# Kernel optimization log

Measured on AMD Instinct MI355X. Metric: run time of the kernel, lower is better.

The kernel has to match this reference:

```python
import jax, jax.numpy as jnp
import numpy as np

N_NODES = 50000
D_FEAT = 128
N_EDGES = 800000
C = 1.0  # curvature (init kwarg)
MIN_NORM = 1e-15
ARTANH_EPS = 1e-15


def logmap0(x, c):
    # PoincareBall.logmap0: x/(sqrt(c)||x||) * artanh(sqrt(c)||x||), with the
    # same clamping as the torch repo (norm clamped to MIN_NORM, artanh arg to 1-eps).
    sqrt_c = c ** 0.5
    x_norm = jnp.maximum(jnp.linalg.norm(x, axis=-1, keepdims=True), MIN_NORM)
    u = jnp.clip(sqrt_c * x_norm, -1.0 + ARTANH_EPS, 1.0 - ARTANH_EPS)
    return x * (jnp.arctanh(u) / (sqrt_c * x_norm))


def setup_inputs() -> dict:
    key = jax.random.key(0)
    k1, k2, k3, k4 = jax.random.split(key, 4)
    # scale into the Poincare ball (||x|| < 1/sqrt(c))
    x = jax.random.normal(k1, (N_NODES, D_FEAT), dtype=jnp.float32) * 1e-3
    adj_rows = jax.random.randint(k2, (N_EDGES,), 0, N_NODES, dtype=jnp.int32)
    adj_cols = jax.random.randint(k3, (N_EDGES,), 0, N_NODES, dtype=jnp.int32)
    adj_vals = jax.random.uniform(k4, (N_EDGES,), dtype=jnp.float32)
    return {"x": x, "adj_rows": adj_rows, "adj_cols": adj_cols, "adj_vals": adj_vals}


def reference(x, adj_rows, adj_cols, adj_vals) -> jnp.ndarray:
    x_tangent = logmap0(x, C)                       # [N, d] elementwise hyperbolic map
    gathered = adj_vals[:, None] * x_tangent[adj_cols]  # [E, d] edge-parallel gather
    support_t = jax.ops.segment_sum(gathered, adj_rows, num_segments=N_NODES)  # [N, d]
    return support_t
```

## Files before the change

kernel.cpp:

```cpp
#include <hip/hip_runtime.h>
#include <math.h>

#define D_FEAT 128
#define CAP 64
#define OCAP 1024

static __device__ inline unsigned short f2bf(float f) {
    unsigned u = __float_as_uint(f);
    u += 0x7FFFu + ((u >> 16) & 1u);
    return (unsigned short)(u >> 16);
}

__global__ void scatter_scale_kernel(const float* __restrict__ x,
                                     unsigned short* __restrict__ xt,
                                     const int* __restrict__ rows,
                                     const int* __restrict__ cols,
                                     const float* __restrict__ vals,
                                     int* __restrict__ cnt,
                                     int2* __restrict__ buckets,
                                     int* __restrict__ ocount,
                                     int4* __restrict__ oedges,
                                     int n_nodes, int n_edges,
                                     int n_scatter_blocks) {
    if ((int)blockIdx.x < n_scatter_blocks) {
        const int xcd = blockIdx.x & 7;
        const int chunk = blockIdx.x >> 3;
        int base = chunk * 1024 + threadIdx.x;
        #pragma unroll
        for (int k = 0; k < 4; ++k) {
            int e = base + k * 256;
            if (e < n_edges) {
                int r = rows[e];
                if ((r & 7) == xcd) {
                    int slot = atomicAdd(&cnt[r], 1);
                    int2 p;
                    p.x = cols[e];
                    p.y = __float_as_int(vals[e]);
                    if (slot < CAP) {
                        buckets[(size_t)r * CAP + slot] = p;
                    } else {
                        int o = atomicAdd(ocount, 1);
                        if (o < OCAP) {
                            int4 q; q.x = r; q.y = p.x; q.z = p.y; q.w = 0;
                            oedges[o] = q;
                        }
                    }
                }
            }
        }
    } else {
        const int lane = threadIdx.x & 63;
        const int wave = threadIdx.x >> 6;
        const int row = ((int)blockIdx.x - n_scatter_blocks) * 4 + wave;
        if (row >= n_nodes) return;

        const float2* xr = (const float2*)(x + (size_t)row * D_FEAT);
        float2 v = xr[lane];
        float ss = v.x * v.x + v.y * v.y;
        #pragma unroll
        for (int off = 32; off > 0; off >>= 1)
            ss += __shfl_xor(ss, off, 64);

        float norm = sqrtf(ss);
        float nc = fmaxf(norm, 1e-15f);
        float u = fminf(nc, 1.0f - 1e-15f);
        float at = 0.5f * (log1pf(u) - log1pf(-u));
        float s = at / nc;

        ushort2 o;
        o.x = f2bf(v.x * s);
        o.y = f2bf(v.y * s);
        ((ushort2*)(xt + (size_t)row * D_FEAT))[lane] = o;
    }
}

__global__ void gather_bucket_kernel(const unsigned short* __restrict__ xt,
                                     const int* __restrict__ cnt,
                                     const int2* __restrict__ buckets,
                                     float* __restrict__ out, int n_nodes) {
    const int lane = threadIdx.x & 63;
    const int wave = threadIdx.x >> 6;
    const int xcd = blockIdx.x & 7;
    const int idx = blockIdx.x >> 3;
    const int m = idx * 4 + wave;
    const int row = xcd + (m << 3);
    if (row >= n_nodes) return;

    int deg = cnt[row];
    deg = deg < CAP ? deg : CAP;

    int2 myp = {0, 0};
    if (lane < deg) myp = buckets[(size_t)row * CAP + lane];
    int pc = myp.x;
    float pw = __int_as_float(myp.y);

    float accx = 0.0f, accy = 0.0f;
    int j = 0;
    for (; j + 8 <= deg; j += 8) {
        int c0 = __shfl(pc, j, 64),     c1 = __shfl(pc, j + 1, 64);
        int c2 = __shfl(pc, j + 2, 64), c3 = __shfl(pc, j + 3, 64);
        int c4 = __shfl(pc, j + 4, 64), c5 = __shfl(pc, j + 5, 64);
        int c6 = __shfl(pc, j + 6, 64), c7 = __shfl(pc, j + 7, 64);
        float w0 = __shfl(pw, j, 64),     w1 = __shfl(pw, j + 1, 64);
        float w2 = __shfl(pw, j + 2, 64), w3 = __shfl(pw, j + 3, 64);
        float w4 = __shfl(pw, j + 4, 64), w5 = __shfl(pw, j + 5, 64);
        float w6 = __shfl(pw, j + 6, 64), w7 = __shfl(pw, j + 7, 64);
        unsigned u0 = ((const unsigned*)(xt + ((size_t)c0 << 7)))[lane];
        unsigned u1 = ((const unsigned*)(xt + ((size_t)c1 << 7)))[lane];
        unsigned u2 = ((const unsigned*)(xt + ((size_t)c2 << 7)))[lane];
        unsigned u3 = ((const unsigned*)(xt + ((size_t)c3 << 7)))[lane];
        unsigned u4 = ((const unsigned*)(xt + ((size_t)c4 << 7)))[lane];
        unsigned u5 = ((const unsigned*)(xt + ((size_t)c5 << 7)))[lane];
        unsigned u6 = ((const unsigned*)(xt + ((size_t)c6 << 7)))[lane];
        unsigned u7 = ((const unsigned*)(xt + ((size_t)c7 << 7)))[lane];
        accx = fmaf(w0, __uint_as_float(u0 << 16), accx);
        accy = fmaf(w0, __uint_as_float(u0 & 0xFFFF0000u), accy);
        accx = fmaf(w1, __uint_as_float(u1 << 16), accx);
        accy = fmaf(w1, __uint_as_float(u1 & 0xFFFF0000u), accy);
        accx = fmaf(w2, __uint_as_float(u2 << 16), accx);
        accy = fmaf(w2, __uint_as_float(u2 & 0xFFFF0000u), accy);
        accx = fmaf(w3, __uint_as_float(u3 << 16), accx);
        accy = fmaf(w3, __uint_as_float(u3 & 0xFFFF0000u), accy);
        accx = fmaf(w4, __uint_as_float(u4 << 16), accx);
        accy = fmaf(w4, __uint_as_float(u4 & 0xFFFF0000u), accy);
        accx = fmaf(w5, __uint_as_float(u5 << 16), accx);
        accy = fmaf(w5, __uint_as_float(u5 & 0xFFFF0000u), accy);
        accx = fmaf(w6, __uint_as_float(u6 << 16), accx);
        accy = fmaf(w6, __uint_as_float(u6 & 0xFFFF0000u), accy);
        accx = fmaf(w7, __uint_as_float(u7 << 16), accx);
        accy = fmaf(w7, __uint_as_float(u7 & 0xFFFF0000u), accy);
    }
    for (; j + 4 <= deg; j += 4) {
        int c0 = __shfl(pc, j, 64),     c1 = __shfl(pc, j + 1, 64);
        int c2 = __shfl(pc, j + 2, 64), c3 = __shfl(pc, j + 3, 64);
        float w0 = __shfl(pw, j, 64),     w1 = __shfl(pw, j + 1, 64);
        float w2 = __shfl(pw, j + 2, 64), w3 = __shfl(pw, j + 3, 64);
        unsigned u0 = ((const unsigned*)(xt + ((size_t)c0 << 7)))[lane];
        unsigned u1 = ((const unsigned*)(xt + ((size_t)c1 << 7)))[lane];
        unsigned u2 = ((const unsigned*)(xt + ((size_t)c2 << 7)))[lane];
        unsigned u3 = ((const unsigned*)(xt + ((size_t)c3 << 7)))[lane];
        accx = fmaf(w0, __uint_as_float(u0 << 16), accx);
        accy = fmaf(w0, __uint_as_float(u0 & 0xFFFF0000u), accy);
        accx = fmaf(w1, __uint_as_float(u1 << 16), accx);
        accy = fmaf(w1, __uint_as_float(u1 & 0xFFFF0000u), accy);
        accx = fmaf(w2, __uint_as_float(u2 << 16), accx);
        accy = fmaf(w2, __uint_as_float(u2 & 0xFFFF0000u), accy);
        accx = fmaf(w3, __uint_as_float(u3 << 16), accx);
        accy = fmaf(w3, __uint_as_float(u3 & 0xFFFF0000u), accy);
    }
    for (; j < deg; ++j) {
        int c = __shfl(pc, j, 64);
        float w = __shfl(pw, j, 64);
        unsigned u = ((const unsigned*)(xt + ((size_t)c << 7)))[lane];
        accx = fmaf(w, __uint_as_float(u << 16), accx);
        accy = fmaf(w, __uint_as_float(u & 0xFFFF0000u), accy);
    }

    float2 o;
    o.x = accx;
    o.y = accy;
    ((float2*)(out + ((size_t)row << 7)))[lane] = o;
}

__global__ void cleanup_kernel(const unsigned short* __restrict__ xt,
                               const int* __restrict__ ocount,
                               const int4* __restrict__ oedges,
                               float* __restrict__ out) {
    int t = blockIdx.x * blockDim.x + threadIdx.x;
    int e = t >> 5, sub = t & 31;
    int n = *ocount;
    n = n < OCAP ? n : OCAP;
    if (e >= n) return;
    int4 q = oedges[e];
    float w = __int_as_float(q.z);
    const unsigned* xr = (const unsigned*)(xt + ((size_t)q.y << 7));
    unsigned u0 = xr[sub * 2], u1 = xr[sub * 2 + 1];
    float* o = out + ((size_t)q.x << 7) + sub * 4;
    atomicAdd(o + 0, w * __uint_as_float(u0 << 16));
    atomicAdd(o + 1, w * __uint_as_float(u0 & 0xFFFF0000u));
    atomicAdd(o + 2, w * __uint_as_float(u1 << 16));
    atomicAdd(o + 3, w * __uint_as_float(u1 & 0xFFFF0000u));
}

__global__ void fallback_kernel(const float* __restrict__ x,
                                const int* __restrict__ rows,
                                const int* __restrict__ cols,
                                const float* __restrict__ vals,
                                float* __restrict__ out, int n_edges) {
    int gid = blockIdx.x * blockDim.x + threadIdx.x;
    int e = gid >> 5, t = gid & 31;
    if (e >= n_edges) return;
    int c = cols[e];
    const float* xr = x + (size_t)c * D_FEAT;
    float ss = 0.0f;
    for (int i = 0; i < D_FEAT; ++i) ss += xr[i] * xr[i];
    float nc = fmaxf(sqrtf(ss), 1e-15f);
    float u = fminf(nc, 1.0f - 1e-15f);
    float w = vals[e] * (0.5f * (log1pf(u) - log1pf(-u))) / nc;
    const float4* xc = (const float4*)xr;
    float4 xv = xc[t];
    float* o = out + (size_t)rows[e] * D_FEAT + t * 4;
    atomicAdd(o + 0, w * xv.x);
    atomicAdd(o + 1, w * xv.y);
    atomicAdd(o + 2, w * xv.z);
    atomicAdd(o + 3, w * xv.w);
}


extern "C" void kernel_launch(void* const* d_in, const int* in_sizes, int n_in,
                              void* d_out, int out_size, void* d_ws, size_t ws_size,
                              hipStream_t stream) {
    const float* x    = (const float*)d_in[0];
    const int*   rows = (const int*)d_in[1];
    const int*   cols = (const int*)d_in[2];
    const float* vals = (const float*)d_in[3];
    float* out = (float*)d_out;

    const int n_nodes = in_sizes[0] / D_FEAT;
    const int n_edges = in_sizes[1];

    char* wsb = (char*)d_ws;
    const int n_chunks = (n_edges + 1023) / 1024;
    const int n_scatter_blocks = 8 * n_chunks;
    const int n_scale_blocks = (n_nodes + 3) / 4;

    size_t xt_bytes    = (size_t)n_nodes * D_FEAT * 2;
    size_t cnt_off     = xt_bytes;
    size_t ocount_off  = cnt_off + (size_t)n_nodes * 4;
    size_t oedges_off  = (ocount_off + 4 + 255) & ~(size_t)255;
    size_t buckets_off = (oedges_off + (size_t)OCAP * 16 + 511) & ~(size_t)511;
    size_t need        = buckets_off + (size_t)n_nodes * CAP * 8;

    if (ws_size >= need) {
        unsigned short* xt = (unsigned short*)wsb;
        int*  cnt     = (int*)(wsb + cnt_off);
        int*  ocount  = (int*)(wsb + ocount_off);
        int4* oedges  = (int4*)(wsb + oedges_off);
        int2* buckets = (int2*)(wsb + buckets_off);

        hipMemsetAsync(cnt, 0, ocount_off + 4 - cnt_off, stream);
        scatter_scale_kernel<<<n_scatter_blocks + n_scale_blocks, 256, 0, stream>>>(
            x, xt, rows, cols, vals, cnt, buckets, ocount, oedges,
            n_nodes, n_edges, n_scatter_blocks);
        {
            int mmax = (n_nodes + 7) >> 3;
            int grid = 8 * ((mmax + 3) / 4);
            gather_bucket_kernel<<<grid, 256, 0, stream>>>(xt, cnt, buckets,
                                                           out, n_nodes);
        }
        cleanup_kernel<<<(OCAP * 32) / 256, 256, 0, stream>>>(xt, ocount, oedges, out);
    } else {
        hipMemsetAsync(out, 0, (size_t)out_size * sizeof(float), stream);
        long long total = (long long)n_edges * 32;
        fallback_kernel<<<(int)((total + 255) / 256), 256, 0, stream>>>(
            x, rows, cols, vals, out, n_edges);
    }
}
```

Baseline: 168.0 us.

## Use persistent XCC-aware work-stealing scatter and vectorized 16B gather loads

Replaces the static scatter grid with a persistent kernel of fixed block count. Each block reads its hardware XCC id and pulls edge chunks from per-partition atomic job counters, so atomics to a row partition tend to stay on one XCD's L2. The node scaling work is interleaved as a separate job queue. The gather kernel now has each 16-lane group load a whole 256B bf16 row with uint4 loads, processing four neighbors per wave per step, then reducing across groups with shuffles. The overflow capacity is also raised. The cost is extra global atomics for job dispatch and reliance on the XCC_ID hardware register.

```diff
diff --git a/kernel.cpp b/kernel.cpp
--- a/kernel.cpp
+++ b/kernel.cpp
@@ -3,7 +3,9 @@
 
 #define D_FEAT 128
 #define CAP 64
-#define OCAP 1024
+#define OCAP 4096
+#define EPJ 1024
+#define GRID_BLOCKS 2048
 
 static __device__ inline unsigned short f2bf(float f) {
     unsigned u = __float_as_uint(f);
@@ -11,79 +13,96 @@
     return (unsigned short)(u >> 16);
 }
 
-__global__ void scatter_scale_kernel(const float* __restrict__ x,
-                                     unsigned short* __restrict__ xt,
-                                     const int* __restrict__ rows,
-                                     const int* __restrict__ cols,
-                                     const float* __restrict__ vals,
-                                     int* __restrict__ cnt,
-                                     int2* __restrict__ buckets,
-                                     int* __restrict__ ocount,
-                                     int4* __restrict__ oedges,
-                                     int n_nodes, int n_edges,
-                                     int n_scatter_blocks) {
-    if ((int)blockIdx.x < n_scatter_blocks) {
-        const int xcd = blockIdx.x & 7;
-        const int chunk = blockIdx.x >> 3;
-        int base = chunk * 1024 + threadIdx.x;
-        #pragma unroll
-        for (int k = 0; k < 4; ++k) {
-            int e = base + k * 256;
-            if (e < n_edges) {
-                int r = rows[e];
-                if ((r & 7) == xcd) {
-                    int slot = atomicAdd(&cnt[r], 1);
-                    int2 p;
-                    p.x = cols[e];
-                    p.y = __float_as_int(vals[e]);
-                    if (slot < CAP) {
-                        buckets[(size_t)r * CAP + slot] = p;
-                    } else {
-                        int o = atomicAdd(ocount, 1);
-                        if (o < OCAP) {
-                            int4 q; q.x = r; q.y = p.x; q.z = p.y; q.w = 0;
-                            oedges[o] = q;
+
+__global__ void __launch_bounds__(256)
+fused_scatter_scale(const float* __restrict__ x,
+                    unsigned short* __restrict__ xt,
+                    const int* __restrict__ rows,
+                    const int* __restrict__ cols,
+                    const float* __restrict__ vals,
+                    int* __restrict__ cnt,
+                    int2* __restrict__ buckets,
+                    int* __restrict__ ctrl,
+                    int4* __restrict__ oedges,
+                    int n_nodes, int n_edges,
+                    int n_chunks, int n_scale_jobs) {
+    __shared__ int s_job;
+    unsigned xcc;
+    asm volatile("s_getreg_b32 %0, hwreg(HW_REG_XCC_ID, 0, 32)" : "=s"(xcc));
+    const int myp = (int)(xcc & 7u);
+
+    for (int d = 0; d < 8; ++d) {
+        if (d == 1) {
+            while (true) {
+                if (threadIdx.x == 0) s_job = atomicAdd(&ctrl[8], 1);
+                __syncthreads();
+                int s = s_job;
+                __syncthreads();
+                if (s >= n_scale_jobs) break;
+                const int lane = threadIdx.x & 63;
+                const int wave = threadIdx.x >> 6;
+                const int row = s * 4 + wave;
+                if (row < n_nodes) {
+                    const float2* xr = (const float2*)(x + (size_t)row * D_FEAT);
+                    float2 v = xr[lane];
+                    float ss = v.x * v.x + v.y * v.y;
+                    #pragma unroll
+                    for (int off = 32; off > 0; off >>= 1)
+                        ss += __shfl_xor(ss, off, 64);
+                    float norm = sqrtf(ss);
+                    float nc = fmaxf(norm, 1e-15f);
+                    float u = fminf(nc, 1.0f - 1e-15f);
+                    float at = 0.5f * (log1pf(u) - log1pf(-u));
+                    float sc = at / nc;
+                    ushort2 o;
+                    o.x = f2bf(v.x * sc);
+                    o.y = f2bf(v.y * sc);
+                    ((ushort2*)(xt + (size_t)row * D_FEAT))[lane] = o;
+                }
+            }
+        }
+        const int q = (myp + d) & 7;
+        while (true) {
+            if (threadIdx.x == 0) s_job = atomicAdd(&ctrl[q], 1);
+            __syncthreads();
+            int c = s_job;
+            __syncthreads();
+            if (c >= n_chunks) break;
+            int base = c * EPJ + threadIdx.x;
+            #pragma unroll
+            for (int k = 0; k < 4; ++k) {
+                int e = base + k * 256;
+                if (e < n_edges) {
+                    int r = rows[e];
+                    if ((r & 7) == q) {
+                        int slot = atomicAdd(&cnt[r], 1);
+                        int2 p;
+                        p.x = cols[e];
+                        p.y = __float_as_int(vals[e]);
+                        if (slot < CAP) {
+                            buckets[(size_t)r * CAP + slot] = p;
+                        } else {
+                            int o = atomicAdd(&ctrl[9], 1);
+                            if (o < OCAP) {
+                                int4 qq; qq.x = r; qq.y = p.x; qq.z = p.y; qq.w = 0;
+                                oedges[o] = qq;
+                            }
                         }
                     }
                 }
             }
         }
-    } else {
-        const int lane = threadIdx.x & 63;
-        const int wave = threadIdx.x >> 6;
-        const int row = ((int)blockIdx.x - n_scatter_blocks) * 4 + wave;
-        if (row >= n_nodes) return;
-
-        const float2* xr = (const float2*)(x + (size_t)row * D_FEAT);
-        float2 v = xr[lane];
-        float ss = v.x * v.x + v.y * v.y;
-        #pragma unroll
-        for (int off = 32; off > 0; off >>= 1)
-            ss += __shfl_xor(ss, off, 64);
-
-        float norm = sqrtf(ss);
-        float nc = fmaxf(norm, 1e-15f);
-        float u = fminf(nc, 1.0f - 1e-15f);
-        float at = 0.5f * (log1pf(u) - log1pf(-u));
-        float s = at / nc;
-
-        ushort2 o;
-        o.x = f2bf(v.x * s);
-        o.y = f2bf(v.y * s);
-        ((ushort2*)(xt + (size_t)row * D_FEAT))[lane] = o;
-    }
-}
-
-__global__ void gather_bucket_kernel(const unsigned short* __restrict__ xt,
-                                     const int* __restrict__ cnt,
-                                     const int2* __restrict__ buckets,
-                                     float* __restrict__ out, int n_nodes) {
+    }
+}
+
+__global__ void __launch_bounds__(256)
+gather_bucket_kernel(const unsigned short* __restrict__ xt,
+                     const int* __restrict__ cnt,
+                     const int2* __restrict__ buckets,
+                     float* __restrict__ out, int n_nodes) {
     const int lane = threadIdx.x & 63;
     const int wave = threadIdx.x >> 6;
-    const int xcd = blockIdx.x & 7;
-    const int idx = blockIdx.x >> 3;
-    const int m = idx * 4 + wave;
-    const int row = xcd + (m << 3);
+    const int row = blockIdx.x * 4 + wave;
     if (row >= n_nodes) return;
 
     int deg = cnt[row];
@@ -94,81 +113,66 @@
     int pc = myp.x;
     float pw = __int_as_float(myp.y);
 
-    float accx = 0.0f, accy = 0.0f;
-    int j = 0;
-    for (; j + 8 <= deg; j += 8) {
-        int c0 = __shfl(pc, j, 64),     c1 = __shfl(pc, j + 1, 64);
-        int c2 = __shfl(pc, j + 2, 64), c3 = __shfl(pc, j + 3, 64);
-        int c4 = __shfl(pc, j + 4, 64), c5 = __shfl(pc, j + 5, 64);
-        int c6 = __shfl(pc, j + 6, 64), c7 = __shfl(pc, j + 7, 64);
-        float w0 = __shfl(pw, j, 64),     w1 = __shfl(pw, j + 1, 64);
-        float w2 = __shfl(pw, j + 2, 64), w3 = __shfl(pw, j + 3, 64);
-        float w4 = __shfl(pw, j + 4, 64), w5 = __shfl(pw, j + 5, 64);
-        float w6 = __shfl(pw, j + 6, 64), w7 = __shfl(pw, j + 7, 64);
-        unsigned u0 = ((const unsigned*)(xt + ((size_t)c0 << 7)))[lane];
-        unsigned u1 = ((const unsigned*)(xt + ((size_t)c1 << 7)))[lane];
-        unsigned u2 = ((const unsigned*)(xt + ((size_t)c2 << 7)))[lane];
-        unsigned u3 = ((const unsigned*)(xt + ((size_t)c3 << 7)))[lane];
-        unsigned u4 = ((const unsigned*)(xt + ((size_t)c4 << 7)))[lane];
-        unsigned u5 = ((const unsigned*)(xt + ((size_t)c5 << 7)))[lane];
-        unsigned u6 = ((const unsigned*)(xt + ((size_t)c6 << 7)))[lane];
-        unsigned u7 = ((const unsigned*)(xt + ((size_t)c7 << 7)))[lane];
-        accx = fmaf(w0, __uint_as_float(u0 << 16), accx);
-        accy = fmaf(w0, __uint_as_float(u0 & 0xFFFF0000u), accy);
-        accx = fmaf(w1, __uint_as_float(u1 << 16), accx);
-        accy = fmaf(w1, __uint_as_float(u1 & 0xFFFF0000u), accy);
-        accx = fmaf(w2, __uint_as_float(u2 << 16), accx);
-        accy = fmaf(w2, __uint_as_float(u2 & 0xFFFF0000u), accy);
-        accx = fmaf(w3, __uint_as_float(u3 << 16), accx);
-        accy = fmaf(w3, __uint_as_float(u3 & 0xFFFF0000u), accy);
-        accx = fmaf(w4, __uint_as_float(u4 << 16), accx);
-        accy = fmaf(w4, __uint_as_float(u4 & 0xFFFF0000u), accy);
-        accx = fmaf(w5, __uint_as_float(u5 << 16), accx);
-        accy = fmaf(w5, __uint_as_float(u5 & 0xFFFF0000u), accy);
-        accx = fmaf(w6, __uint_as_float(u6 << 16), accx);
-        accy = fmaf(w6, __uint_as_float(u6 & 0xFFFF0000u), accy);
-        accx = fmaf(w7, __uint_as_float(u7 << 16), accx);
-        accy = fmaf(w7, __uint_as_float(u7 & 0xFFFF0000u), accy);
-    }
-    for (; j + 4 <= deg; j += 4) {
-        int c0 = __shfl(pc, j, 64),     c1 = __shfl(pc, j + 1, 64);
-        int c2 = __shfl(pc, j + 2, 64), c3 = __shfl(pc, j + 3, 64);
-        float w0 = __shfl(pw, j, 64),     w1 = __shfl(pw, j + 1, 64);
-        float w2 = __shfl(pw, j + 2, 64), w3 = __shfl(pw, j + 3, 64);
-        unsigned u0 = ((const unsigned*)(xt + ((size_t)c0 << 7)))[lane];
-        unsigned u1 = ((const unsigned*)(xt + ((size_t)c1 << 7)))[lane];
-        unsigned u2 = ((const unsigned*)(xt + ((size_t)c2 << 7)))[lane];
-        unsigned u3 = ((const unsigned*)(xt + ((size_t)c3 << 7)))[lane];
-        accx = fmaf(w0, __uint_as_float(u0 << 16), accx);
-        accy = fmaf(w0, __uint_as_float(u0 & 0xFFFF0000u), accy);
-        accx = fmaf(w1, __uint_as_float(u1 << 16), accx);
-        accy = fmaf(w1, __uint_as_float(u1 & 0xFFFF0000u), accy);
-        accx = fmaf(w2, __uint_as_float(u2 << 16), accx);
-        accy = fmaf(w2, __uint_as_float(u2 & 0xFFFF0000u), accy);
-        accx = fmaf(w3, __uint_as_float(u3 << 16), accx);
-        accy = fmaf(w3, __uint_as_float(u3 & 0xFFFF0000u), accy);
-    }
-    for (; j < deg; ++j) {
-        int c = __shfl(pc, j, 64);
-        float w = __shfl(pw, j, 64);
-        unsigned u = ((const unsigned*)(xt + ((size_t)c << 7)))[lane];
-        accx = fmaf(w, __uint_as_float(u << 16), accx);
-        accy = fmaf(w, __uint_as_float(u & 0xFFFF0000u), accy);
-    }
-
-    float2 o;
-    o.x = accx;
-    o.y = accy;
-    ((float2*)(out + ((size_t)row << 7)))[lane] = o;
+    const int g = lane >> 4;
+    const int t = lane & 15;
+
+    float a0 = 0, a1 = 0, a2 = 0, a3 = 0, a4 = 0, a5 = 0, a6 = 0, a7 = 0;
+
+    for (int j = 0; j < deg; j += 8) {
+        int i0 = j + g, i1 = j + 4 + g;
+        int i0c = i0 < deg ? i0 : 0;
+        int i1c = i1 < deg ? i1 : 0;
+        int c0 = __shfl(pc, i0c, 64);
+        int c1 = __shfl(pc, i1c, 64);
+        float w0 = __shfl(pw, i0c, 64);
+        float w1 = __shfl(pw, i1c, 64);
+        if (i0 >= deg) w0 = 0.0f;
+        if (i1 >= deg) w1 = 0.0f;
+        uint4 u0 = ((const uint4*)(xt + ((size_t)c0 << 7)))[t];
+        uint4 u1 = ((const uint4*)(xt + ((size_t)c1 << 7)))[t];
+        a0 = fmaf(w0, __uint_as_float(u0.x << 16), a0);
+        a1 = fmaf(w0, __uint_as_float(u0.x & 0xFFFF0000u), a1);
+        a2 = fmaf(w0, __uint_as_float(u0.y << 16), a2);
+        a3 = fmaf(w0, __uint_as_float(u0.y & 0xFFFF0000u), a3);
+        a4 = fmaf(w0, __uint_as_float(u0.z << 16), a4);
+        a5 = fmaf(w0, __uint_as_float(u0.z & 0xFFFF0000u), a5);
+        a6 = fmaf(w0, __uint_as_float(u0.w << 16), a6);
+        a7 = fmaf(w0, __uint_as_float(u0.w & 0xFFFF0000u), a7);
+        a0 = fmaf(w1, __uint_as_float(u1.x << 16), a0);
+        a1 = fmaf(w1, __uint_as_float(u1.x & 0xFFFF0000u), a1);
+        a2 = fmaf(w1, __uint_as_float(u1.y << 16), a2);
+        a3 = fmaf(w1, __uint_as_float(u1.y & 0xFFFF0000u), a3);
+        a4 = fmaf(w1, __uint_as_float(u1.z << 16), a4);
+        a5 = fmaf(w1, __uint_as_float(u1.z & 0xFFFF0000u), a5);
+        a6 = fmaf(w1, __uint_as_float(u1.w << 16), a6);
+        a7 = fmaf(w1, __uint_as_float(u1.w & 0xFFFF0000u), a7);
+    }
+
+    a0 += __shfl_xor(a0, 16, 64); a0 += __shfl_xor(a0, 32, 64);
+    a1 += __shfl_xor(a1, 16, 64); a1 += __shfl_xor(a1, 32, 64);
+    a2 += __shfl_xor(a2, 16, 64); a2 += __shfl_xor(a2, 32, 64);
+    a3 += __shfl_xor(a3, 16, 64); a3 += __shfl_xor(a3, 32, 64);
+    a4 += __shfl_xor(a4, 16, 64); a4 += __shfl_xor(a4, 32, 64);
+    a5 += __shfl_xor(a5, 16, 64); a5 += __shfl_xor(a5, 32, 64);
+    a6 += __shfl_xor(a6, 16, 64); a6 += __shfl_xor(a6, 32, 64);
+    a7 += __shfl_xor(a7, 16, 64); a7 += __shfl_xor(a7, 32, 64);
+
+    if (g == 0) {
+        float4* op = (float4*)(out + ((size_t)row << 7) + t * 8);
+        float4 o0; o0.x = a0; o0.y = a1; o0.z = a2; o0.w = a3;
+        float4 o1; o1.x = a4; o1.y = a5; o1.z = a6; o1.w = a7;
+        op[0] = o0;
+        op[1] = o1;
+    }
 }
 
 __global__ void cleanup_kernel(const unsigned short* __restrict__ xt,
-                               const int* __restrict__ ocount,
+                               const int* __restrict__ ctrl,
                                const int4* __restrict__ oedges,
                                float* __restrict__ out) {
-    int t = blockIdx.x * blockDim.x + threadIdx.x;
-    int e = t >> 5, sub = t & 31;
-    int n = *ocount;
+    int tt = blockIdx.x * blockDim.x + threadIdx.x;
+    int e = tt >> 5, sub = tt & 31;
+    int n = ctrl[9];
     n = n < OCAP ? n : OCAP;
     if (e >= n) return;
     int4 q = oedges[e];
@@ -220,35 +224,30 @@
     const int n_edges = in_sizes[1];
 
     char* wsb = (char*)d_ws;
-    const int n_chunks = (n_edges + 1023) / 1024;
-    const int n_scatter_blocks = 8 * n_chunks;
-    const int n_scale_blocks = (n_nodes + 3) / 4;
+    const int n_chunks = (n_edges + EPJ - 1) / EPJ;
+    const int n_scale_jobs = (n_nodes + 3) / 4;
 
     size_t xt_bytes    = (size_t)n_nodes * D_FEAT * 2;
     size_t cnt_off     = xt_bytes;
-    size_t ocount_off  = cnt_off + (size_t)n_nodes * 4;
-    size_t oedges_off  = (ocount_off + 4 + 255) & ~(size_t)255;
+    size_t ctrl_off    = cnt_off + (size_t)n_nodes * 4;
+    size_t oedges_off  = (ctrl_off + 64 + 255) & ~(size_t)255;
     size_t buckets_off = (oedges_off + (size_t)OCAP * 16 + 511) & ~(size_t)511;
     size_t need        = buckets_off + (size_t)n_nodes * CAP * 8;
 
     if (ws_size >= need) {
         unsigned short* xt = (unsigned short*)wsb;
         int*  cnt     = (int*)(wsb + cnt_off);
-        int*  ocount  = (int*)(wsb + ocount_off);
+        int*  ctrl    = (int*)(wsb + ctrl_off);
         int4* oedges  = (int4*)(wsb + oedges_off);
         int2* buckets = (int2*)(wsb + buckets_off);
 
-        hipMemsetAsync(cnt, 0, ocount_off + 4 - cnt_off, stream);
-        scatter_scale_kernel<<<n_scatter_blocks + n_scale_blocks, 256, 0, stream>>>(
-            x, xt, rows, cols, vals, cnt, buckets, ocount, oedges,
-            n_nodes, n_edges, n_scatter_blocks);
-        {
-            int mmax = (n_nodes + 7) >> 3;
-            int grid = 8 * ((mmax + 3) / 4);
-            gather_bucket_kernel<<<grid, 256, 0, stream>>>(xt, cnt, buckets,
-                                                           out, n_nodes);
-        }
-        cleanup_kernel<<<(OCAP * 32) / 256, 256, 0, stream>>>(xt, ocount, oedges, out);
+        hipMemsetAsync(cnt, 0, (ctrl_off + 64) - cnt_off, stream);
+        fused_scatter_scale<<<GRID_BLOCKS, 256, 0, stream>>>(
+            x, xt, rows, cols, vals, cnt, buckets, ctrl, oedges,
+            n_nodes, n_edges, n_chunks, n_scale_jobs);
+        gather_bucket_kernel<<<(n_nodes + 3) / 4, 256, 0, stream>>>(
+            xt, cnt, buckets, out, n_nodes);
+        cleanup_kernel<<<(OCAP * 32) / 256, 256, 0, stream>>>(xt, ctrl, oedges, out);
     } else {
         hipMemsetAsync(out, 0, (size_t)out_size * sizeof(float), stream);
         long long total = (long long)n_edges * 32;
```

Measured after the change: 545.6 us. +224.8%, slower.
